# Kernel optimization log

Measured on AMD Instinct MI355X. Metric: run time of the kernel, lower is better.

Reference implementation:

```python
import jax, jax.numpy as jnp
import numpy as np

NEG_FILL = -1e4  # finite stand-in for -inf so sort/cumsum stay NaN-free


def entmax15(X):
    """1.5-entmax along the last axis (Peters et al. 2019, sort-based exact algorithm)."""
    X = X - jnp.max(X, axis=-1, keepdims=True)
    X = X * 0.5  # alpha=1.5 transform
    Xsrt = -jnp.sort(-X, axis=-1)  # descending sort
    S = X.shape[-1]
    rho = jnp.arange(1, S + 1, dtype=X.dtype)  # 1..S support-size candidates
    mean = jnp.cumsum(Xsrt, axis=-1) / rho
    mean_sq = jnp.cumsum(Xsrt * Xsrt, axis=-1) / rho
    ss = rho * (mean_sq - mean * mean)          # running k*variance
    delta = (1.0 - ss) / rho
    tau = mean - jnp.sqrt(jnp.clip(delta, 0.0, None))
    support_size = jnp.sum(tau <= Xsrt, axis=-1, keepdims=True)
    tau_star = jnp.take_along_axis(tau, support_size - 1, axis=-1)
    return jnp.square(jnp.clip(X - tau_star, 0.0, None))


def setup_inputs() -> dict:
    key = jax.random.key(0)
    k1, k2 = jax.random.split(key)
    B, S = 32768, 2048
    scores = jax.random.normal(k1, (B, S), dtype=jnp.float32)
    mask = jax.random.randint(k2, (B, S), 0, 2, dtype=jnp.int32)
    mask = mask.at[:, 0].set(1)  # guarantee at least one unmasked token per row
    return {"scores": scores, "mask": mask}


def reference(scores, mask):
    # replace_masked_values(scores, mask, -inf) -> entmax15(dim=-1)
    masked_scores = jnp.where(mask.astype(bool), scores, NEG_FILL)
    return entmax15(masked_scores)
```

## Files before the change

kernel.cpp:

```cpp
#include <hip/hip_runtime.h>


#define NEG_FILL (-1.0e4f)

static constexpr int S_DIM = 2048;
static constexpr int WAVES_PER_BLOCK = 4;
static constexpr int ELEMS = S_DIM / 64;
static constexpr int VEC = ELEMS / 4;

__global__ __launch_bounds__(256) void entmax15_kernel(
    const float* __restrict__ scores,
    const int*   __restrict__ mask,
    float*       __restrict__ out,
    int nrows)
{
    const int lane = threadIdx.x & 63;
    const int wave = threadIdx.x >> 6;
    const int row  = blockIdx.x * WAVES_PER_BLOCK + wave;
    if (row >= nrows) return;

    const size_t base = (size_t)row * S_DIM;
    const float4* __restrict__ srow = (const float4*)(scores + base);
    const int4*   __restrict__ mrow = (const int4*)(mask + base);
    float4*       __restrict__ orow = (float4*)(out + base);

    float x[ELEMS];
    float rmax = -3.402823466e38f;
#pragma unroll
    for (int j = 0; j < VEC; ++j) {
        const float4 s = srow[lane + 64 * j];
        const int4   m = mrow[lane + 64 * j];
        float v0 = m.x ? s.x : NEG_FILL;
        float v1 = m.y ? s.y : NEG_FILL;
        float v2 = m.z ? s.z : NEG_FILL;
        float v3 = m.w ? s.w : NEG_FILL;
        x[4 * j + 0] = v0;
        x[4 * j + 1] = v1;
        x[4 * j + 2] = v2;
        x[4 * j + 3] = v3;
        rmax = fmaxf(rmax, fmaxf(fmaxf(v0, v1), fmaxf(v2, v3)));
    }
#pragma unroll
    for (int off = 32; off >= 1; off >>= 1)
        rmax = fmaxf(rmax, __shfl_xor(rmax, off, 64));

    const float shift = -0.5f * rmax;
#pragma unroll
    for (int i = 0; i < ELEMS; ++i)
        x[i] = fmaf(0.5f, x[i], shift);

    float tau = -1.0f;
#pragma unroll 1
    for (int it = 0; it < 16; ++it) {
        float F = 0.0f, G = 0.0f, K = 0.0f;
#pragma unroll
        for (int i = 0; i < ELEMS; ++i) {
            float d = x[i] - tau;
            float y = fmaxf(d, 0.0f);
            F = fmaf(y, y, F);
            G += y;
            K += (d > 0.0f) ? 1.0f : 0.0f;
        }
#pragma unroll
        for (int off = 32; off >= 1; off >>= 1) {
            F += __shfl_xor(F, off, 64);
            G += __shfl_xor(G, off, 64);
            K += __shfl_xor(K, off, 64);
        }
        const float c = F - 1.0f;
        const float disc = fmaf(G, G, -K * c);
        const float denom = (disc > 0.0f) ? (G + sqrtf(disc)) : (2.0f * G);
        const float u = c / denom;
        tau += u;
        if (!(fabsf(u) > 2e-7f)) break;
    }

#pragma unroll
    for (int j = 0; j < VEC; ++j) {
        float y0 = fmaxf(x[4 * j + 0] - tau, 0.0f);
        float y1 = fmaxf(x[4 * j + 1] - tau, 0.0f);
        float y2 = fmaxf(x[4 * j + 2] - tau, 0.0f);
        float y3 = fmaxf(x[4 * j + 3] - tau, 0.0f);
        float4 o;
        o.x = y0 * y0;
        o.y = y1 * y1;
        o.z = y2 * y2;
        o.w = y3 * y3;
        orow[lane + 64 * j] = o;
    }
}

extern "C" void kernel_launch(void* const* d_in, const int* in_sizes, int n_in,
                              void* d_out, int out_size, void* d_ws, size_t ws_size,
                              hipStream_t stream) {
    const float* scores = (const float*)d_in[0];
    const int*   mask   = (const int*)d_in[1];
    float*       out    = (float*)d_out;

    const int nrows = in_sizes[0] / S_DIM;
    const int grid  = (nrows + WAVES_PER_BLOCK - 1) / WAVES_PER_BLOCK;

    entmax15_kernel<<<grid, 256, 0, stream>>>(scores, mask, out, nrows);
}
```

Before: 586.4 us.

## Vectorize entmax Newton loop with packed float2, ballot counts, fused first iteration

Rewrites the per-row Newton iteration using two-wide float vectors so the compiler can emit packed FMA/max/add, and replaces the float count reduction with wave ballot plus popcount, which removes one shuffle reduction per iteration. The scaling pass is fused with the first Newton iteration. Output writes become nontemporal stores. These changes aim to cut VALU and cross-lane work in a compute-heavy loop, at the cost of extra scalar popcount work per element pair.

```diff
diff --git a/kernel.cpp b/kernel.cpp
--- a/kernel.cpp
+++ b/kernel.cpp
@@ -3,10 +3,14 @@
 
 #define NEG_FILL (-1.0e4f)
 
+typedef float float2v __attribute__((ext_vector_type(2)));
+typedef float float4v __attribute__((ext_vector_type(4)));
+
 static constexpr int S_DIM = 2048;
 static constexpr int WAVES_PER_BLOCK = 4;
 static constexpr int ELEMS = S_DIM / 64;
 static constexpr int VEC = ELEMS / 4;
+static constexpr int VEC2 = ELEMS / 2;
 
 __global__ __launch_bounds__(256) void entmax15_kernel(
     const float* __restrict__ scores,
@@ -22,7 +26,7 @@
     const size_t base = (size_t)row * S_DIM;
     const float4* __restrict__ srow = (const float4*)(scores + base);
     const int4*   __restrict__ mrow = (const int4*)(mask + base);
-    float4*       __restrict__ orow = (float4*)(out + base);
+    float4v*      __restrict__ orow = (float4v*)(out + base);
 
     float x[ELEMS];
     float rmax = -3.402823466e38f;
@@ -45,48 +49,83 @@
         rmax = fmaxf(rmax, __shfl_xor(rmax, off, 64));
 
     const float shift = -0.5f * rmax;
+    float2v* xv = (float2v*)x;
+
+    const float2v h05  = {0.5f, 0.5f};
+    const float2v sh2  = {shift, shift};
+    const float2v one2 = {1.0f, 1.0f};
+    const float2v zero2 = {0.0f, 0.0f};
+
+    float2v F2 = zero2, G2 = zero2;
+    int K = 0;
 #pragma unroll
-    for (int i = 0; i < ELEMS; ++i)
-        x[i] = fmaf(0.5f, x[i], shift);
+    for (int i = 0; i < VEC2; ++i) {
+        float2v t = __builtin_elementwise_fma(xv[i], h05, sh2);
+        xv[i] = t;
+        float2v d = t + one2;
+        float2v y = __builtin_elementwise_max(d, zero2);
+        F2 = __builtin_elementwise_fma(y, y, F2);
+        G2 = G2 + y;
+        K += __popcll(__ballot(d.x > 0.0f));
+        K += __popcll(__ballot(d.y > 0.0f));
+    }
 
-    float tau = -1.0f;
+    float2v FG;
+    FG.x = F2.x + F2.y;
+    FG.y = G2.x + G2.y;
+#pragma unroll
+    for (int off = 32; off >= 1; off >>= 1) {
+        float2v t;
+        t.x = __shfl_xor(FG.x, off, 64);
+        t.y = __shfl_xor(FG.y, off, 64);
+        FG += t;
+    }
+
+    float c     = FG.x - 1.0f;
+    float disc  = fmaf(FG.y, FG.y, -(float)K * c);
+    float denom = (disc > 0.0f) ? (FG.y + sqrtf(disc)) : (2.0f * FG.y);
+    float u     = c / denom;
+    float tau   = -1.0f + u;
+
 #pragma unroll 1
-    for (int it = 0; it < 16; ++it) {
-        float F = 0.0f, G = 0.0f, K = 0.0f;
+    for (int it = 1; it < 16 && fabsf(u) > 2e-7f; ++it) {
+        const float2v t2 = {tau, tau};
+        F2 = zero2; G2 = zero2; K = 0;
 #pragma unroll
-        for (int i = 0; i < ELEMS; ++i) {
-            float d = x[i] - tau;
-            float y = fmaxf(d, 0.0f);
-            F = fmaf(y, y, F);
-            G += y;
-            K += (d > 0.0f) ? 1.0f : 0.0f;
+        for (int i = 0; i < VEC2; ++i) {
+            float2v d = xv[i] - t2;
+            float2v y = __builtin_elementwise_max(d, zero2);
+            F2 = __builtin_elementwise_fma(y, y, F2);
+            G2 = G2 + y;
+            K += __popcll(__ballot(d.x > 0.0f));
+            K += __popcll(__ballot(d.y > 0.0f));
         }
+        FG.x = F2.x + F2.y;
+        FG.y = G2.x + G2.y;
 #pragma unroll
         for (int off = 32; off >= 1; off >>= 1) {
-            F += __shfl_xor(F, off, 64);
-            G += __shfl_xor(G, off, 64);
-            K += __shfl_xor(K, off, 64);
+            float2v t;
+            t.x = __shfl_xor(FG.x, off, 64);
+            t.y = __shfl_xor(FG.y, off, 64);
+            FG += t;
         }
-        const float c = F - 1.0f;
-        const float disc = fmaf(G, G, -K * c);
-        const float denom = (disc > 0.0f) ? (G + sqrtf(disc)) : (2.0f * G);
-        const float u = c / denom;
-        tau += u;
-        if (!(fabsf(u) > 2e-7f)) break;
+        c     = FG.x - 1.0f;
+        disc  = fmaf(FG.y, FG.y, -(float)K * c);
+        denom = (disc > 0.0f) ? (FG.y + sqrtf(disc)) : (2.0f * FG.y);
+        u     = c / denom;
+        tau  += u;
     }
 
+    const float2v t2 = {tau, tau};
 #pragma unroll
     for (int j = 0; j < VEC; ++j) {
-        float y0 = fmaxf(x[4 * j + 0] - tau, 0.0f);
-        float y1 = fmaxf(x[4 * j + 1] - tau, 0.0f);
-        float y2 = fmaxf(x[4 * j + 2] - tau, 0.0f);
-        float y3 = fmaxf(x[4 * j + 3] - tau, 0.0f);
-        float4 o;
-        o.x = y0 * y0;
-        o.y = y1 * y1;
-        o.z = y2 * y2;
-        o.w = y3 * y3;
-        orow[lane + 64 * j] = o;
+        float2v ya = __builtin_elementwise_max(xv[2 * j]     - t2, zero2);
+        float2v yb = __builtin_elementwise_max(xv[2 * j + 1] - t2, zero2);
+        float2v oa = ya * ya;
+        float2v ob = yb * yb;
+        float4v o;
+        o.x = oa.x; o.y = oa.y; o.z = ob.x; o.w = ob.y;
+        __builtin_nontemporal_store(o, &orow[lane + 64 * j]);
     }
 }
 
```

Measured after the change: 598.6 us. +2.1%, slower.
